# Kernel optimization log

Hardware: AMD Instinct MI355X
Metric: run time of the kernel (lower is better)

Reference implementation:

```python
import jax, jax.numpy as jnp
import numpy as np

BITS = 8
QMAX = float(2 ** (BITS - 1) - 1)  # 127 for 8-bit symmetric


def bits_quant(x):
    """8-bit symmetric per-tensor fake quantization (models the opaque bits_quant op)."""
    max_abs = jnp.max(jnp.abs(x))
    scale = jnp.where(max_abs > 0, max_abs / QMAX, 1.0).astype(x.dtype)
    q = jnp.clip(jnp.round(x / scale), -QMAX, QMAX) * scale
    return q


def quant_linear(x, w, b):
    # Q(Q(x @ w) + Q(b)) then Q of the result, per QuantLinearLayer.call
    y = bits_quant(jnp.matmul(x, w)) + bits_quant(b)
    return bits_quant(y)


def setup_inputs() -> dict:
    d = 4096
    key = jax.random.key(0)
    ks = jax.random.split(key, 12)
    s = 0.02
    return {
        "inputs": jax.random.normal(ks[0], (1, d), dtype=jnp.float32),
        "c": jax.random.normal(ks[1], (1, d), dtype=jnp.float32) * s,
        "h": jax.random.normal(ks[2], (1, d), dtype=jnp.float32) * s,
        "Wf_w": jax.random.normal(ks[3], (2 * d, d), dtype=jnp.float32) * s,
        "Wf_b": jax.random.normal(ks[4], (d,), dtype=jnp.float32) * s,
        "Wi_w": jax.random.normal(ks[5], (2 * d, d), dtype=jnp.float32) * s,
        "Wi_b": jax.random.normal(ks[6], (d,), dtype=jnp.float32) * s,
        "Wc_w": jax.random.normal(ks[7], (2 * d, d), dtype=jnp.float32) * s,
        "Wc_b": jax.random.normal(ks[8], (d,), dtype=jnp.float32) * s,
        "Wo_w": jax.random.normal(ks[9], (2 * d, d), dtype=jnp.float32) * s,
        "Wo_b": jax.random.normal(ks[10], (d,), dtype=jnp.float32) * s,
    }


def reference(inputs, c, h, Wf_w, Wf_b, Wi_w, Wi_b, Wc_w, Wc_b, Wo_w, Wo_b):
    # concat = Q([h, x])  -> [1, 2d]
    concat = bits_quant(jnp.concatenate([h, inputs], axis=1))
    z = bits_quant(jnp.tanh(quant_linear(concat, Wc_w, Wc_b)))
    zf = bits_quant(jax.nn.sigmoid(quant_linear(concat, Wf_w, Wf_b)))
    zi = bits_quant(jax.nn.sigmoid(quant_linear(concat, Wi_w, Wi_b)))
    zo = bits_quant(jax.nn.sigmoid(quant_linear(concat, Wo_w, Wo_b)))
    memory = bits_quant(z * zi)
    c_new = bits_quant(bits_quant(c * zf) + memory)
    h_new = bits_quant(zo * bits_quant(jnp.tanh(c_new)))
    return h_new
```

## Files before the change

### kernel.cpp

```cpp
#include <hip/hip_runtime.h>
#include <math.h>

#define QMAXF 127.0f

struct Ptrs4 { const float* p[4]; };

__device__ __forceinline__ float qscale(float m) {
    return (m > 0.0f) ? (m / QMAXF) : 1.0f;
}

__device__ __forceinline__ float quant1(float x, float s) {
    float r = rintf(x / s);
    r = fminf(fmaxf(r, -QMAXF), QMAXF);
    return r * s;
}

__device__ __forceinline__ float block_max_red(float v, float* sred) {
    #pragma unroll
    for (int off = 32; off > 0; off >>= 1)
        v = fmaxf(v, __shfl_down(v, off, 64));
    int wave = threadIdx.x >> 6;
    int lane = threadIdx.x & 63;
    __syncthreads();
    if (lane == 0) sred[wave] = v;
    __syncthreads();
    if (threadIdx.x == 0) {
        int nw = blockDim.x >> 6;
        float m = sred[0];
        for (int i = 1; i < nw; ++i) m = fmaxf(m, sred[i]);
        sred[16] = m;
    }
    __syncthreads();
    return sred[16];
}

__device__ __forceinline__ void quant_vec4(float* a, float* sred) {
    float pm = 0.0f;
    #pragma unroll
    for (int i = 0; i < 4; ++i) pm = fmaxf(pm, fabsf(a[i]));
    float s = qscale(block_max_red(pm, sred));
    #pragma unroll
    for (int i = 0; i < 4; ++i) a[i] = quant1(a[i], s);
}

__global__ __launch_bounds__(1024) void k_prep(
    const float* __restrict__ x, const float* __restrict__ h,
    Ptrs4 biases, float* __restrict__ concat_q, float* __restrict__ qb,
    unsigned* __restrict__ gmax)
{
    __shared__ float sred[17];
    int tid = threadIdx.x;
    if (blockIdx.x == 0) {
        if (tid < 4) gmax[tid] = 0u;
        float vals[8];
        float pm = 0.0f;
        #pragma unroll
        for (int i = 0; i < 8; ++i) {
            int idx = i * 1024 + tid;
            float v = (i < 4) ? h[idx] : x[idx - 4096];
            vals[i] = v;
            pm = fmaxf(pm, fabsf(v));
        }
        float s = qscale(block_max_red(pm, sred));
        #pragma unroll
        for (int i = 0; i < 8; ++i) concat_q[i * 1024 + tid] = quant1(vals[i], s);
    } else {
        int g = blockIdx.x - 1;
        const float* __restrict__ b = biases.p[g];
        float vals[4];
        float pm = 0.0f;
        #pragma unroll
        for (int i = 0; i < 4; ++i) {
            float v = b[i * 1024 + tid];
            vals[i] = v;
            pm = fmaxf(pm, fabsf(v));
        }
        float s = qscale(block_max_red(pm, sred));
        #pragma unroll
        for (int i = 0; i < 4; ++i) qb[g * 4096 + i * 1024 + tid] = quant1(vals[i], s);
    }
}

__global__ __launch_bounds__(256, 2) void k_gemv(
    Ptrs4 wts, const float* __restrict__ xq, float* __restrict__ partials)
{
    __shared__ float ring[4][8 * 512];
    __shared__ float x_s[256];

    int ct = blockIdx.x;
    int kc = blockIdx.y;
    int g  = blockIdx.z;
    const float* __restrict__ W = wts.p[g];
    int tid  = threadIdx.x;
    int wave = tid >> 6;
    int lane = tid & 63;
    int k0 = kc * 256;
    const float* __restrict__ wbase = W + (size_t)k0 * 4096 + ct * 512;

    auto stage = [&](int st) {
        const float* wsrc = wbase + (size_t)(st * 8) * 4096;
        float* lbuf = &ring[st & 3][0];
        #pragma unroll
        for (int j = 0; j < 4; ++j) {
            int t = wave * 4 + j;
            int row = t >> 1, half = t & 1;
            __builtin_amdgcn_global_load_lds(
                (const __attribute__((address_space(1))) void*)
                    (wsrc + (size_t)row * 4096 + half * 256 + lane * 4),
                (__attribute__((address_space(3))) void*)
                    (lbuf + row * 512 + half * 256), 16, 0, 0);
        }
    };

    float ax = 0.f, ay = 0.f;

    auto compute = [&](int t) {
        const float* sl = &ring[t & 3][0];
        int kb = t * 8;
        #pragma unroll
        for (int r = 0; r < 8; ++r) {
            float xv = x_s[kb + r];
            float2 wv = *(const float2*)&sl[r * 512 + tid * 2];
            ax = fmaf(xv, wv.x, ax);
            ay = fmaf(xv, wv.y, ay);
        }
    };

    #define WAITBAR(N) asm volatile("s_waitcnt vmcnt(" #N ") lgkmcnt(0)\ns_barrier" ::: "memory")

    x_s[tid] = xq[k0 + tid];
    __syncthreads();
    stage(0); stage(1); stage(2);

    for (int t = 0; t < 30; ++t) {
        WAITBAR(8);
        compute(t);
        if (t + 3 < 32) stage(t + 3);
    }
    WAITBAR(4);
    compute(30);
    WAITBAR(0);
    compute(31);
    #undef WAITBAR

    int col0 = ct * 512 + tid * 2;
    float2 r; r.x = ax; r.y = ay;
    *(float2*)(partials + (size_t)(g * 32 + kc) * 4096 + col0) = r;
}

__global__ __launch_bounds__(256) void k_reduce(
    const float* __restrict__ partials, float* __restrict__ y,
    unsigned* __restrict__ gmax)
{
    int g  = blockIdx.x >> 4;
    int cb = blockIdx.x & 15;
    int col = cb * 256 + threadIdx.x;
    float s = 0.0f;
    #pragma unroll 8
    for (int kc = 0; kc < 32; ++kc)
        s += partials[(size_t)(g * 32 + kc) * 4096 + col];
    y[g * 4096 + col] = s;

    float m = fabsf(s);
    #pragma unroll
    for (int off = 32; off > 0; off >>= 1)
        m = fmaxf(m, __shfl_down(m, off, 64));
    __shared__ float sm[4];
    int wave = threadIdx.x >> 6, lane = threadIdx.x & 63;
    if (lane == 0) sm[wave] = m;
    __syncthreads();
    if (threadIdx.x == 0) {
        float mm = fmaxf(fmaxf(sm[0], sm[1]), fmaxf(sm[2], sm[3]));
        atomicMax(gmax + g, __float_as_uint(mm));
    }
}

__global__ __launch_bounds__(1024) void k_epilogue(
    const float* __restrict__ y, const float* __restrict__ qb,
    const unsigned* __restrict__ gmax, const float* __restrict__ c,
    float* __restrict__ out)
{
    __shared__ float sred[17];
    int tid = threadIdx.x;
    float v[4][4];

    #pragma unroll
    for (int g = 0; g < 4; ++g) {
        float s = qscale(__uint_as_float(gmax[g]));
        #pragma unroll
        for (int i = 0; i < 4; ++i) {
            int col = i * 1024 + tid;
            v[g][i] = quant1(y[g * 4096 + col], s) + qb[g * 4096 + col];
        }
    }

    for (int g = 0; g < 4; ++g) {
        float pm = 0.0f;
        #pragma unroll
        for (int i = 0; i < 4; ++i) pm = fmaxf(pm, fabsf(v[g][i]));
        float s = qscale(block_max_red(pm, sred));
        #pragma unroll
        for (int i = 0; i < 4; ++i) {
            float q = quant1(v[g][i], s);
            v[g][i] = (g == 2) ? tanhf(q) : (1.0f / (1.0f + expf(-q)));
        }
    }

    for (int g = 0; g < 4; ++g) {
        float pm = 0.0f;
        #pragma unroll
        for (int i = 0; i < 4; ++i) pm = fmaxf(pm, fabsf(v[g][i]));
        float s = qscale(block_max_red(pm, sred));
        #pragma unroll
        for (int i = 0; i < 4; ++i) v[g][i] = quant1(v[g][i], s);
    }

    float mem[4];
    #pragma unroll
    for (int i = 0; i < 4; ++i) mem[i] = v[2][i] * v[1][i];
    quant_vec4(mem, sred);

    float cf[4];
    #pragma unroll
    for (int i = 0; i < 4; ++i) cf[i] = c[i * 1024 + tid] * v[0][i];
    quant_vec4(cf, sred);

    float cn[4];
    #pragma unroll
    for (int i = 0; i < 4; ++i) cn[i] = cf[i] + mem[i];
    quant_vec4(cn, sred);

    float tc[4];
    #pragma unroll
    for (int i = 0; i < 4; ++i) tc[i] = tanhf(cn[i]);
    quant_vec4(tc, sred);

    float hn[4];
    #pragma unroll
    for (int i = 0; i < 4; ++i) hn[i] = v[3][i] * tc[i];
    quant_vec4(hn, sred);
    #pragma unroll
    for (int i = 0; i < 4; ++i) out[i * 1024 + tid] = hn[i];
}

extern "C" void kernel_launch(void* const* d_in, const int* in_sizes, int n_in,
                              void* d_out, int out_size, void* d_ws, size_t ws_size,
                              hipStream_t stream) {
    const float* x = (const float*)d_in[0];
    const float* c = (const float*)d_in[1];
    const float* h = (const float*)d_in[2];
    Ptrs4 wts, bs;
    wts.p[0] = (const float*)d_in[3];  bs.p[0] = (const float*)d_in[4];
    wts.p[1] = (const float*)d_in[5];  bs.p[1] = (const float*)d_in[6];
    wts.p[2] = (const float*)d_in[7];  bs.p[2] = (const float*)d_in[8];
    wts.p[3] = (const float*)d_in[9];  bs.p[3] = (const float*)d_in[10];

    float* ws = (float*)d_ws;
    float* partials = ws;
    float* concat_q = ws + 524288;
    float* qb       = ws + 532480;
    float* yv       = ws + 548864;
    unsigned* gmax  = (unsigned*)(ws + 565248);

    hipLaunchKernelGGL(k_prep,     dim3(5),        dim3(1024), 0, stream,
                       x, h, bs, concat_q, qb, gmax);
    hipLaunchKernelGGL(k_gemv,     dim3(8, 32, 4), dim3(256),  0, stream,
                       wts, concat_q, partials);
    hipLaunchKernelGGL(k_reduce,   dim3(64),       dim3(256),  0, stream,
                       partials, yv, gmax);
    hipLaunchKernelGGL(k_epilogue, dim3(1),        dim3(1024), 0, stream,
                       yv, qb, gmax, c, (float*)d_out);
}
```

Measured before the change: 479.9 us.

## Split GEMV into full-row-strip blocks with direct float4 loads and two-level reduction

Replaces the LDS-staged GEMV with a kernel where each block handles 32 contiguous rows across all 4096 columns, reading weights straight into registers as float4. That gives fully contiguous 16 KB row reads and 1024 blocks for more memory-level parallelism. The cost is a much larger partial buffer (about 16 MB written, then read back), so an extra k_mid reduction kernel and another launch are added. The old path is kept as a fallback for when the workspace is too small.

After: 486.1 us. No clear change (+1.3%).

```diff
diff --git a/kernel.cpp b/kernel.cpp
--- a/kernel.cpp
+++ b/kernel.cpp
@@ -81,15 +81,73 @@
     }
 }
 
-__global__ __launch_bounds__(256, 2) void k_gemv(
+__global__ __launch_bounds__(256, 4) void k_gemv_rows(
+    Ptrs4 wts, const float* __restrict__ xq, float* __restrict__ partials)
+{
+    __shared__ float x_s[32];
+    int chunk = blockIdx.x;
+    int g     = blockIdx.y;
+    int tid   = threadIdx.x;
+    int wave  = tid >> 6;
+    int lane  = tid & 63;
+    int r0    = chunk * 32;
+
+    if (tid < 32) x_s[tid] = xq[r0 + tid];
+    __syncthreads();
+
+    int colbase = wave * 1024 + lane * 4;
+    const float* __restrict__ wp = wts.p[g] + (size_t)r0 * 4096 + colbase;
+
+    float4 a0 = {0.f,0.f,0.f,0.f}, a1 = {0.f,0.f,0.f,0.f};
+    float4 a2 = {0.f,0.f,0.f,0.f}, a3 = {0.f,0.f,0.f,0.f};
+
+    #pragma unroll
+    for (int r = 0; r < 32; ++r) {
+        const float* rp = wp + (size_t)r * 4096;
+        float xv = x_s[r];
+        float4 w0 = *(const float4*)(rp);
+        float4 w1 = *(const float4*)(rp + 256);
+        float4 w2 = *(const float4*)(rp + 512);
+        float4 w3 = *(const float4*)(rp + 768);
+        a0.x = fmaf(xv, w0.x, a0.x); a0.y = fmaf(xv, w0.y, a0.y);
+        a0.z = fmaf(xv, w0.z, a0.z); a0.w = fmaf(xv, w0.w, a0.w);
+        a1.x = fmaf(xv, w1.x, a1.x); a1.y = fmaf(xv, w1.y, a1.y);
+        a1.z = fmaf(xv, w1.z, a1.z); a1.w = fmaf(xv, w1.w, a1.w);
+        a2.x = fmaf(xv, w2.x, a2.x); a2.y = fmaf(xv, w2.y, a2.y);
+        a2.z = fmaf(xv, w2.z, a2.z); a2.w = fmaf(xv, w2.w, a2.w);
+        a3.x = fmaf(xv, w3.x, a3.x); a3.y = fmaf(xv, w3.y, a3.y);
+        a3.z = fmaf(xv, w3.z, a3.z); a3.w = fmaf(xv, w3.w, a3.w);
+    }
+
+    float* out = partials + (size_t)(g * 256 + chunk) * 4096 + colbase;
+    *(float4*)(out)       = a0;
+    *(float4*)(out + 256) = a1;
+    *(float4*)(out + 512) = a2;
+    *(float4*)(out + 768) = a3;
+}
+
+__global__ __launch_bounds__(256) void k_mid(
+    const float* __restrict__ pbig, float* __restrict__ psmall)
+{
+    int cb = blockIdx.x, s = blockIdx.y, g = blockIdx.z;
+    int col = cb * 1024 + threadIdx.x * 4;
+    const float* __restrict__ base = pbig + (size_t)(g * 256 + s * 8) * 4096 + col;
+    float4 acc = *(const float4*)(base);
+    #pragma unroll
+    for (int j = 1; j < 8; ++j) {
+        float4 v = *(const float4*)(base + (size_t)j * 4096);
+        acc.x += v.x; acc.y += v.y; acc.z += v.z; acc.w += v.w;
+    }
+    *(float4*)(psmall + (size_t)(g * 32 + s) * 4096 + col) = acc;
+}
+
+__global__ __launch_bounds__(256, 2) void k_gemv_fb(
     Ptrs4 wts, const float* __restrict__ xq, float* __restrict__ partials)
 {
     __shared__ float ring[4][8 * 512];
     __shared__ float x_s[256];
 
-    int ct = blockIdx.x;
-    int kc = blockIdx.y;
-    int g  = blockIdx.z;
+    int ct = blockIdx.x, kc = blockIdx.y, g = blockIdx.z;
     const float* __restrict__ W = wts.p[g];
     int tid  = threadIdx.x;
     int wave = tid >> 6;
@@ -113,7 +171,6 @@
     };
 
     float ax = 0.f, ay = 0.f;
-
     auto compute = [&](int t) {
         const float* sl = &ring[t & 3][0];
         int kb = t * 8;
@@ -127,11 +184,9 @@
     };
 
     #define WAITBAR(N) asm volatile("s_waitcnt vmcnt(" #N ") lgkmcnt(0)\ns_barrier" ::: "memory")
-
     x_s[tid] = xq[k0 + tid];
     __syncthreads();
     stage(0); stage(1); stage(2);
-
     for (int t = 0; t < 30; ++t) {
         WAITBAR(8);
         compute(t);
@@ -256,18 +311,43 @@
     wts.p[3] = (const float*)d_in[9];  bs.p[3] = (const float*)d_in[10];
 
     float* ws = (float*)d_ws;
-    float* partials = ws;
-    float* concat_q = ws + 524288;
-    float* qb       = ws + 532480;
-    float* yv       = ws + 548864;
-    unsigned* gmax  = (unsigned*)(ws + 565248);
-
-    hipLaunchKernelGGL(k_prep,     dim3(5),        dim3(1024), 0, stream,
-                       x, h, bs, concat_q, qb, gmax);
-    hipLaunchKernelGGL(k_gemv,     dim3(8, 32, 4), dim3(256),  0, stream,
-                       wts, concat_q, partials);
-    hipLaunchKernelGGL(k_reduce,   dim3(64),       dim3(256),  0, stream,
-                       partials, yv, gmax);
-    hipLaunchKernelGGL(k_epilogue, dim3(1),        dim3(1024), 0, stream,
-                       yv, qb, gmax, c, (float*)d_out);
-}
+
+    const size_t PBIG = 4u * 256u * 4096u;
+    const size_t PSM  = 4u * 32u * 4096u;
+    const size_t NEED = (PBIG + PSM + 8192 + 16384 + 16384 + 16) * sizeof(float);
+
+    if (ws_size >= NEED) {
+        float* pbig     = ws;
+        float* psmall   = ws + PBIG;
+        float* concat_q = ws + PBIG + PSM;
+        float* qb       = concat_q + 8192;
+        float* yv       = qb + 16384;
+        unsigned* gmax  = (unsigned*)(yv + 16384);
+
+        hipLaunchKernelGGL(k_prep,      dim3(5),         dim3(1024), 0, stream,
+                           x, h, bs, concat_q, qb, gmax);
+        hipLaunchKernelGGL(k_gemv_rows, dim3(256, 4),    dim3(256),  0, stream,
+                           wts, concat_q, pbig);
+        hipLaunchKernelGGL(k_mid,       dim3(4, 32, 4),  dim3(256),  0, stream,
+                           pbig, psmall);
+        hipLaunchKernelGGL(k_reduce,    dim3(64),        dim3(256),  0, stream,
+                           psmall, yv, gmax);
+        hipLaunchKernelGGL(k_epilogue,  dim3(1),         dim3(1024), 0, stream,
+                           yv, qb, gmax, c, (float*)d_out);
+    } else {
+        float* partials = ws;
+        float* concat_q = ws + 524288;
+        float* qb       = ws + 532480;
+        float* yv       = ws + 548864;
+        unsigned* gmax  = (unsigned*)(ws + 565248);
+
+        hipLaunchKernelGGL(k_prep,     dim3(5),        dim3(1024), 0, stream,
+                           x, h, bs, concat_q, qb, gmax);
+        hipLaunchKernelGGL(k_gemv_fb,  dim3(8, 32, 4), dim3(256),  0, stream,
+                           wts, concat_q, partials);
+        hipLaunchKernelGGL(k_reduce,   dim3(64),       dim3(256),  0, stream,
+                           partials, yv, gmax);
+        hipLaunchKernelGGL(k_epilogue, dim3(1),        dim3(1024), 0, stream,
+                           yv, qb, gmax, c, (float*)d_out);
+    }
+}
```
